# Kernel optimization log

Measured on AMD Instinct MI355X. Metric: run time of the kernel, lower is better.

The kernel has to match this reference:

```python
import jax, jax.numpy as jnp
import numpy as np


@jax.custom_vjp
def binarize(w):
    # Deterministic binarization: sign with ties (w==0) mapped to +1,
    # matching tf.where(w >= 0, 1.0, -1.0).
    return jnp.where(w >= 0, 1.0, -1.0).astype(w.dtype)


def _binarize_fwd(w):
    return binarize(w), w


def _binarize_bwd(w, g):
    # Straight-through estimator: pass grad where |w| < 1, else 0.
    return (jnp.where(jnp.abs(w) < 1.0, g, jnp.zeros_like(g)),)


binarize.defvjp(_binarize_fwd, _binarize_bwd)


def setup_inputs() -> dict:
    key = jax.random.key(0)
    kx, kw = jax.random.split(key)
    # NHWC activations
    x = jax.random.normal(kx, (32, 112, 112, 128), dtype=jnp.float32)
    # HWIO kernel (glorot-scale init so values straddle the +/- decision boundary)
    kernel = jax.random.normal(kw, (3, 3, 128, 256), dtype=jnp.float32) * 0.05
    return {"x": x, "kernel": kernel}


def reference(x, kernel):
    wb = binarize(kernel)  # [3,3,Cin,Cout] in {-1,+1}
    return jax.lax.conv_general_dilated(
        x, wb,
        window_strides=(1, 1),
        padding="SAME",
        dimension_numbers=("NHWC", "HWIO", "NHWC"),
    )
```

## Files before the change

### kernel.cpp

```cpp
#include <hip/hip_runtime.h>

typedef __attribute__((ext_vector_type(8))) short short8;
typedef __attribute__((ext_vector_type(4))) float f32x4;
typedef __attribute__((ext_vector_type(4))) unsigned short u16x4;
typedef __attribute__((ext_vector_type(8))) unsigned short u16x8;

#define H 112
#define W 112
#define HP 114
#define WP 114
#define CIN 128
#define COUT 256
#define NPIX (H * W)
#define NIMG 32
#define MTOT (NIMG * NPIX)
#define PADELEMS ((long)NIMG * HP * WP * CIN)
#define NKT 18

__device__ __forceinline__ unsigned short f2bf(float f) {
    unsigned int u = __builtin_bit_cast(unsigned int, f);
    u += 0x7FFFu + ((u >> 16) & 1u);
    return (unsigned short)(u >> 16);
}

__device__ __forceinline__ void gl2lds16(const void* g, void* l) {
    __builtin_amdgcn_global_load_lds(
        (const __attribute__((address_space(1))) unsigned int*)g,
        (__attribute__((address_space(3))) unsigned int*)l,
        16, 0, 0);
}

__global__ void binw2_kernel(const float* __restrict__ kw, unsigned short* __restrict__ bw) {
    int tid = blockIdx.x * 256 + threadIdx.x;
    int c    = tid & 63;
    int cout = (tid >> 6) & 255;
    int kh   = (tid >> 14) & 1;
    int tap  = tid >> 15;
    int cin  = kh * 64 + c;
    float w = kw[(tap * 128 + cin) * 256 + cout];
    bw[tid] = (w >= 0.0f) ? (unsigned short)0x3F80u : (unsigned short)0xBF80u;
}

__global__ void pad_kernel(const float* __restrict__ x, unsigned short* __restrict__ xp) {
    long tid = (long)blockIdx.x * 256 + threadIdx.x;
    if (tid >= PADELEMS / 8) return;
    int c8 = (int)(tid & 15);
    long rem = tid >> 4;
    int wp = (int)(rem % WP); rem /= WP;
    int hp = (int)(rem % HP);
    int n  = (int)(rem / HP);
    u16x8 v = {0, 0, 0, 0, 0, 0, 0, 0};
    if (hp >= 1 && hp <= H && wp >= 1 && wp <= W) {
        const float* s = x + (((long)(n * H + hp - 1) * W + (wp - 1)) * CIN + c8 * 8);
        f32x4 a = *(const f32x4*)s;
        f32x4 b = *(const f32x4*)(s + 4);
        v = (u16x8){ f2bf(a.x), f2bf(a.y), f2bf(a.z), f2bf(a.w),
                     f2bf(b.x), f2bf(b.y), f2bf(b.z), f2bf(b.w) };
    }
    *(u16x8*)(xp + tid * 8) = v;
}

__global__ __launch_bounds__(512, 2)
void conv3_kernel(const unsigned short* __restrict__ xp, const unsigned short* __restrict__ bw,
                  float* __restrict__ out) {
    __shared__ unsigned short As[2][256 * 64];
    __shared__ unsigned short Bs[2][256 * 64];

    const int tid = threadIdx.x;
    const int bm = (blockIdx.x & 7) * 196 + (blockIdx.x >> 3);
    const int lane = tid & 63;
    const int wv = tid >> 6;
    const int wr = wv >> 2;
    const int wc = wv & 3;

    const int r0 = tid >> 3;
    const int c8 = (tid & 7) ^ (r0 & 7);
    long apix[4];
#pragma unroll
    for (int j = 0; j < 4; ++j) {
        int row = r0 + j * 64;
        int p = bm * 256 + row;
        int n = p / NPIX;
        int rem = p - n * NPIX;
        int oh = rem / W, ow = rem - oh * W;
        apix[j] = (long)((n * HP + oh + 1) * WP + (ow + 1)) * CIN;
    }

#define STAGE(T1, BUF) do {                                                     \
        const int _tap = (T1) >> 1, _kh = (T1) & 1;                             \
        const long _sh = (long)((_tap / 3 - 1) * WP + (_tap % 3 - 1)) * CIN     \
                         + _kh * 64 + c8 * 8;                                   \
        const unsigned short* _bb = bw + ((_tap * 2 + _kh) << 14)               \
                                    + r0 * 64 + c8 * 8;                         \
        _Pragma("unroll")                                                       \
        for (int j = 0; j < 4; ++j)                                             \
            gl2lds16(xp + apix[j] + _sh, &As[BUF][(j * 512 + wv * 64) * 8]);    \
        _Pragma("unroll")                                                       \
        for (int j = 0; j < 4; ++j)                                             \
            gl2lds16(_bb + j * 4096, &Bs[BUF][(j * 512 + wv * 64) * 8]);        \
    } while (0)

    const int l15 = lane & 15;
    const int lq16 = (lane >> 4) * 16;
    const int arow0 = wr * 128 + l15;
    const int aswz = (arow0 & 7) << 4;
    const int abase = arow0 * 128 + lq16;
    const int brow0 = wc * 64 + l15;
    const int bswz = (brow0 & 7) << 4;
    const int bbase = brow0 * 128 + lq16;

    f32x4 acc[8][4];
#pragma unroll
    for (int m = 0; m < 8; ++m)
#pragma unroll
        for (int n = 0; n < 4; ++n)
            acc[m][n] = (f32x4){0.f, 0.f, 0.f, 0.f};

    STAGE(0, 0);

    short8 bfrag[4][2];
    for (int t = 0; t < NKT; ++t) {
        const int cur = t & 1;
        if (t < NKT - 1) {
            STAGE(t + 1, cur ^ 1);
            asm volatile("s_waitcnt vmcnt(8)" ::: "memory");
        } else {
            asm volatile("s_waitcnt vmcnt(0)" ::: "memory");
        }
        __builtin_amdgcn_s_barrier();

        const char* ab = (const char*)&As[cur][0];
        const char* bb = (const char*)&Bs[cur][0];
#pragma unroll
        for (int p = 0; p < 4; ++p) {
            if (p == 0) {
#pragma unroll
                for (int n = 0; n < 4; ++n)
#pragma unroll
                    for (int kk = 0; kk < 2; ++kk)
                        bfrag[n][kk] = *(const short8*)(bb + ((bbase + n * 2048 + kk * 64) ^ bswz));
            }
            short8 afr[2][2];
#pragma unroll
            for (int mi = 0; mi < 2; ++mi)
#pragma unroll
                for (int kk = 0; kk < 2; ++kk)
                    afr[mi][kk] = *(const short8*)(ab + ((abase + (2 * p + mi) * 2048 + kk * 64) ^ aswz));

            __builtin_amdgcn_s_setprio(1);
#pragma unroll
            for (int mi = 0; mi < 2; ++mi)
#pragma unroll
                for (int n = 0; n < 4; ++n)
#pragma unroll
                    for (int kk = 0; kk < 2; ++kk)
                        acc[2 * p + mi][n] = __builtin_amdgcn_mfma_f32_16x16x32_bf16(
                            afr[mi][kk], bfrag[n][kk], acc[2 * p + mi][n], 0, 0, 0);
            __builtin_amdgcn_s_setprio(0);
            __builtin_amdgcn_s_barrier();
        }
    }
#undef STAGE

    const long row0 = (long)bm * 256 + wr * 128 + (lane >> 4) * 4;
    const int col = wc * 64 + (lane & 15);
#pragma unroll
    for (int m = 0; m < 8; ++m)
#pragma unroll
        for (int n = 0; n < 4; ++n)
#pragma unroll
            for (int j = 0; j < 4; ++j)
                out[(row0 + m * 16 + j) * COUT + col + n * 16] = acc[m][n][j];
}

__global__ void binw_kernel(const float* __restrict__ kw, unsigned short* __restrict__ bw) {
    int tid = blockIdx.x * 256 + threadIdx.x;
    int cin5 = tid & 31;
    int cout = (tid >> 5) & 255;
    int kc4  = (tid >> 13) & 3;
    int tap  = tid >> 15;
    int cin  = kc4 * 32 + cin5;
    float w = kw[(tap * 128 + cin) * 256 + cout];
    bw[tid] = (w >= 0.0f) ? (unsigned short)0x3F80u : (unsigned short)0xBF80u;
}

__global__ __launch_bounds__(256, 2)
void conv_fallback_kernel(const float* __restrict__ x, const unsigned short* __restrict__ bw,
                          float* __restrict__ out) {
    __shared__ unsigned short As[128][40];
    __shared__ unsigned short Bs[128][40];
    const int tid = threadIdx.x;
    const int bm = blockIdx.x, bn = blockIdx.y;
    const int lane = tid & 63;
    const int wv = tid >> 6;
    const int wr = wv >> 1, wc = wv & 1;
    const int c4 = (tid & 7) * 4;
    const int rseg = tid >> 3;
    int ohs[4], ows[4], bases[4];
#pragma unroll
    for (int i = 0; i < 4; ++i) {
        int p = bm * 128 + rseg + i * 32;
        int n = p / NPIX;
        int rem = p - n * NPIX;
        int oh = rem / W, ow = rem - oh * W;
        ohs[i] = oh; ows[i] = ow;
        bases[i] = ((n * H + oh) * W + ow) * CIN;
    }
    f32x4 acc[4][4];
#pragma unroll
    for (int m = 0; m < 4; ++m)
#pragma unroll
        for (int n = 0; n < 4; ++n)
            acc[m][n] = (f32x4){0.f, 0.f, 0.f, 0.f};
    const int arow = wr * 64 + (lane & 15);
    const int brow = wc * 64 + (lane & 15);
    const int koff = (lane >> 4) * 8;
    for (int tap = 0; tap < 9; ++tap) {
        const int dh = tap / 3 - 1, dw = tap % 3 - 1;
        const int shift = (dh * W + dw) * CIN;
#pragma unroll
        for (int kc = 0; kc < 4; ++kc) {
            __syncthreads();
#pragma unroll
            for (int i = 0; i < 4; ++i) {
                int ih = ohs[i] + dh, iw = ows[i] + dw;
                bool valid = ((unsigned)ih < (unsigned)H) & ((unsigned)iw < (unsigned)W);
                f32x4 v = {0.f, 0.f, 0.f, 0.f};
                if (valid) v = *(const f32x4*)(x + bases[i] + shift + kc * 32 + c4);
                u16x4 s = { f2bf(v.x), f2bf(v.y), f2bf(v.z), f2bf(v.w) };
                *(u16x4*)&As[rseg + i * 32][c4] = s;
            }
            const unsigned short* bp = bw + tap * 32768 + kc * 8192 + bn * 4096;
#pragma unroll
            for (int j = 0; j < 2; ++j) {
                int idx = tid + j * 256;
                *(u16x8*)&Bs[idx >> 2][(idx & 3) * 8] = *(const u16x8*)(bp + (idx >> 2) * 32 + (idx & 3) * 8);
            }
            __syncthreads();
            short8 af[4], bfr[4];
#pragma unroll
            for (int m = 0; m < 4; ++m)
                af[m] = *(const short8*)&As[arow + m * 16][koff];
#pragma unroll
            for (int n = 0; n < 4; ++n)
                bfr[n] = *(const short8*)&Bs[brow + n * 16][koff];
#pragma unroll
            for (int m = 0; m < 4; ++m)
#pragma unroll
                for (int n = 0; n < 4; ++n)
                    acc[m][n] = __builtin_amdgcn_mfma_f32_16x16x32_bf16(af[m], bfr[n], acc[m][n], 0, 0, 0);
        }
    }
    const long row0 = (long)bm * 128 + wr * 64 + ((lane >> 4) * 4);
    const int col = bn * 128 + wc * 64 + (lane & 15);
#pragma unroll
    for (int m = 0; m < 4; ++m)
#pragma unroll
        for (int n = 0; n < 4; ++n)
#pragma unroll
            for (int j = 0; j < 4; ++j)
                out[(row0 + m * 16 + j) * COUT + col + n * 16] = acc[m][n][j];
}

extern "C" void kernel_launch(void* const* d_in, const int* in_sizes, int n_in,
                              void* d_out, int out_size, void* d_ws, size_t ws_size,
                              hipStream_t stream) {
    const float* x  = (const float*)d_in[0];
    const float* kw = (const float*)d_in[1];
    float* out = (float*)d_out;
    unsigned short* bw = (unsigned short*)d_ws;
    const size_t BW_BYTES = 9 * 2 * 256 * 64 * 2;
    const size_t PAD_BYTES = (size_t)PADELEMS * 2;

    if (ws_size >= BW_BYTES + PAD_BYTES) {
        binw2_kernel<<<(9 * 2 * 256 * 64) / 256, 256, 0, stream>>>(kw, bw);
        unsigned short* xp = (unsigned short*)((char*)d_ws + BW_BYTES);
        pad_kernel<<<(int)((PADELEMS / 8 + 255) / 256), 256, 0, stream>>>(x, xp);
        conv3_kernel<<<MTOT / 256, 512, 0, stream>>>(xp, bw, out);
    } else {
        binw_kernel<<<(9 * 256 * 128) / 256, 256, 0, stream>>>(kw, bw);
        dim3 grid(MTOT / 128, COUT / 128);
        conv_fallback_kernel<<<grid, 256, 0, stream>>>(x, bw, out);
    }
}
```

Before: 395.3 us.

## Interleave next-tile global-to-LDS loads across MFMA sub-phases in conv kernel

Splits the per-iteration prefetch of the next K tile into four quarters, each issued inside one of the four MFMA sub-phases, instead of issuing all loads at the top of the iteration. The last iteration is peeled and runs without prefetch or extra barriers. Explicit lgkmcnt waits and sched_barrier pin down instruction order. The goal is to spread memory traffic and hide load latency behind compute. The risk is extra scheduling constraints and barriers that could stall the waves.

```diff
diff --git a/kernel.cpp b/kernel.cpp
--- a/kernel.cpp
+++ b/kernel.cpp
@@ -61,7 +61,7 @@
 }
 
 __global__ __launch_bounds__(512, 2)
-void conv3_kernel(const unsigned short* __restrict__ xp, const unsigned short* __restrict__ bw,
+void conv4_kernel(const unsigned short* __restrict__ xp, const unsigned short* __restrict__ bw,
                   float* __restrict__ out) {
     __shared__ unsigned short As[2][256 * 64];
     __shared__ unsigned short Bs[2][256 * 64];
@@ -86,18 +86,13 @@
         apix[j] = (long)((n * HP + oh + 1) * WP + (ow + 1)) * CIN;
     }
 
-#define STAGE(T1, BUF) do {                                                     \
+#define STAGE_HALF(T1, BUF, J) do {                                             \
         const int _tap = (T1) >> 1, _kh = (T1) & 1;                             \
         const long _sh = (long)((_tap / 3 - 1) * WP + (_tap % 3 - 1)) * CIN     \
                          + _kh * 64 + c8 * 8;                                   \
-        const unsigned short* _bb = bw + ((_tap * 2 + _kh) << 14)               \
-                                    + r0 * 64 + c8 * 8;                         \
-        _Pragma("unroll")                                                       \
-        for (int j = 0; j < 4; ++j)                                             \
-            gl2lds16(xp + apix[j] + _sh, &As[BUF][(j * 512 + wv * 64) * 8]);    \
-        _Pragma("unroll")                                                       \
-        for (int j = 0; j < 4; ++j)                                             \
-            gl2lds16(_bb + j * 4096, &Bs[BUF][(j * 512 + wv * 64) * 8]);        \
+        gl2lds16(xp + apix[J] + _sh, &As[BUF][((J) * 512 + wv * 64) * 8]);      \
+        gl2lds16(bw + ((_tap * 2 + _kh) << 14) + r0 * 64 + c8 * 8 + (J) * 4096, \
+                 &Bs[BUF][((J) * 512 + wv * 64) * 8]);                          \
     } while (0)
 
     const int l15 = lane & 15;
@@ -116,37 +111,45 @@
         for (int n = 0; n < 4; ++n)
             acc[m][n] = (f32x4){0.f, 0.f, 0.f, 0.f};
 
-    STAGE(0, 0);
-
-    short8 bfrag[4][2];
-    for (int t = 0; t < NKT; ++t) {
+    STAGE_HALF(0, 0, 0);
+    STAGE_HALF(0, 0, 1);
+    STAGE_HALF(0, 0, 2);
+    STAGE_HALF(0, 0, 3);
+
+    for (int t = 0; t < NKT - 1; ++t) {
         const int cur = t & 1;
-        if (t < NKT - 1) {
-            STAGE(t + 1, cur ^ 1);
-            asm volatile("s_waitcnt vmcnt(8)" ::: "memory");
-        } else {
-            asm volatile("s_waitcnt vmcnt(0)" ::: "memory");
-        }
-        __builtin_amdgcn_s_barrier();
-
+        const int nxt = cur ^ 1;
         const char* ab = (const char*)&As[cur][0];
         const char* bb = (const char*)&Bs[cur][0];
+        short8 bfrag[4][2];
 #pragma unroll
         for (int p = 0; p < 4; ++p) {
+            short8 afr[2][2];
             if (p == 0) {
+                STAGE_HALF(t + 1, nxt, 0);
+                asm volatile("s_waitcnt vmcnt(2)" ::: "memory");
+                __builtin_amdgcn_s_barrier();
 #pragma unroll
                 for (int n = 0; n < 4; ++n)
 #pragma unroll
                     for (int kk = 0; kk < 2; ++kk)
                         bfrag[n][kk] = *(const short8*)(bb + ((bbase + n * 2048 + kk * 64) ^ bswz));
+#pragma unroll
+                for (int mi = 0; mi < 2; ++mi)
+#pragma unroll
+                    for (int kk = 0; kk < 2; ++kk)
+                        afr[mi][kk] = *(const short8*)(ab + ((abase + mi * 2048 + kk * 64) ^ aswz));
+            } else {
+#pragma unroll
+                for (int mi = 0; mi < 2; ++mi)
+#pragma unroll
+                    for (int kk = 0; kk < 2; ++kk)
+                        afr[mi][kk] = *(const short8*)(ab + ((abase + (2 * p + mi) * 2048 + kk * 64) ^ aswz));
+                STAGE_HALF(t + 1, nxt, p);
+                __builtin_amdgcn_s_barrier();
             }
-            short8 afr[2][2];
-#pragma unroll
-            for (int mi = 0; mi < 2; ++mi)
-#pragma unroll
-                for (int kk = 0; kk < 2; ++kk)
-                    afr[mi][kk] = *(const short8*)(ab + ((abase + (2 * p + mi) * 2048 + kk * 64) ^ aswz));
-
+            asm volatile("s_waitcnt lgkmcnt(0)" ::: "memory");
+            __builtin_amdgcn_sched_barrier(0);
             __builtin_amdgcn_s_setprio(1);
 #pragma unroll
             for (int mi = 0; mi < 2; ++mi)
@@ -160,7 +163,38 @@
             __builtin_amdgcn_s_barrier();
         }
     }
-#undef STAGE
+
+    {
+        const int cur = (NKT - 1) & 1;
+        const char* ab = (const char*)&As[cur][0];
+        const char* bb = (const char*)&Bs[cur][0];
+        asm volatile("s_waitcnt vmcnt(0)" ::: "memory");
+        __builtin_amdgcn_s_barrier();
+        short8 bfrag[4][2];
+#pragma unroll
+        for (int n = 0; n < 4; ++n)
+#pragma unroll
+            for (int kk = 0; kk < 2; ++kk)
+                bfrag[n][kk] = *(const short8*)(bb + ((bbase + n * 2048 + kk * 64) ^ bswz));
+#pragma unroll
+        for (int p = 0; p < 4; ++p) {
+            short8 afr[2][2];
+#pragma unroll
+            for (int mi = 0; mi < 2; ++mi)
+#pragma unroll
+                for (int kk = 0; kk < 2; ++kk)
+                    afr[mi][kk] = *(const short8*)(ab + ((abase + (2 * p + mi) * 2048 + kk * 64) ^ aswz));
+#pragma unroll
+            for (int mi = 0; mi < 2; ++mi)
+#pragma unroll
+                for (int n = 0; n < 4; ++n)
+#pragma unroll
+                    for (int kk = 0; kk < 2; ++kk)
+                        acc[2 * p + mi][n] = __builtin_amdgcn_mfma_f32_16x16x32_bf16(
+                            afr[mi][kk], bfrag[n][kk], acc[2 * p + mi][n], 0, 0, 0);
+        }
+    }
+#undef STAGE_HALF
 
     const long row0 = (long)bm * 256 + wr * 128 + (lane >> 4) * 4;
     const int col = wc * 64 + (lane & 15);
@@ -276,7 +310,7 @@
         binw2_kernel<<<(9 * 2 * 256 * 64) / 256, 256, 0, stream>>>(kw, bw);
         unsigned short* xp = (unsigned short*)((char*)d_ws + BW_BYTES);
         pad_kernel<<<(int)((PADELEMS / 8 + 255) / 256), 256, 0, stream>>>(x, xp);
-        conv3_kernel<<<MTOT / 256, 512, 0, stream>>>(xp, bw, out);
+        conv4_kernel<<<MTOT / 256, 512, 0, stream>>>(xp, bw, out);
     } else {
         binw_kernel<<<(9 * 256 * 128) / 256, 256, 0, stream>>>(kw, bw);
         dim3 grid(MTOT / 128, COUT / 128);
```

After: 360.1 us. 1.1x faster.

## Switch conv GEMM to 32x32x16 MFMA with k-plane LDS layout

Applied to the files above, without the earlier changes.

Replaces the 16x16x32 bf16 MFMA tiling with 32x32x16 MFMA tiles (4x2 per wave) and reorganizes LDS so each 8-channel slice is stored as its own plane across 256 rows. The intent is to cut LDS fragment reads per MFMA and drop the XOR swizzle in favor of a simpler plane layout, while fully unrolling the K loop and removing the per-subtile barriers and priority hints. It risks LDS bank conflicts from the unswizzled layout and higher register pressure from the fully unrolled loop.

```diff
diff --git a/kernel.cpp b/kernel.cpp
--- a/kernel.cpp
+++ b/kernel.cpp
@@ -2,6 +2,7 @@
 
 typedef __attribute__((ext_vector_type(8))) short short8;
 typedef __attribute__((ext_vector_type(4))) float f32x4;
+typedef __attribute__((ext_vector_type(16))) float f32x16;
 typedef __attribute__((ext_vector_type(4))) unsigned short u16x4;
 typedef __attribute__((ext_vector_type(8))) unsigned short u16x8;
 
@@ -28,6 +29,13 @@
         (const __attribute__((address_space(1))) unsigned int*)g,
         (__attribute__((address_space(3))) unsigned int*)l,
         16, 0, 0);
+}
+
+__device__ __forceinline__ int pidx(int p) {
+    int n = p / NPIX;
+    int r = p - n * NPIX;
+    int oh = r / W, ow = r - oh * W;
+    return n * (HP * WP) + (oh + 1) * WP + ow + 1;
 }
 
 __global__ void binw2_kernel(const float* __restrict__ kw, unsigned short* __restrict__ bw) {
@@ -61,10 +69,10 @@
 }
 
 __global__ __launch_bounds__(512, 2)
-void conv3_kernel(const unsigned short* __restrict__ xp, const unsigned short* __restrict__ bw,
-                  float* __restrict__ out) {
-    __shared__ unsigned short As[2][256 * 64];
-    __shared__ unsigned short Bs[2][256 * 64];
+void conv11_kernel(const unsigned short* __restrict__ xp, const unsigned short* __restrict__ bw,
+                   float* __restrict__ out) {
+    __shared__ unsigned short As[2][8 * 256 * 8];
+    __shared__ unsigned short Bs[2][8 * 256 * 8];
 
     const int tid = threadIdx.x;
     const int bm = (blockIdx.x & 7) * 196 + (blockIdx.x >> 3);
@@ -72,105 +80,86 @@
     const int wv = tid >> 6;
     const int wr = wv >> 2;
     const int wc = wv & 3;
-
-    const int r0 = tid >> 3;
-    const int c8 = (tid & 7) ^ (r0 & 7);
-    long apix[4];
-#pragma unroll
-    for (int j = 0; j < 4; ++j) {
-        int row = r0 + j * 64;
-        int p = bm * 256 + row;
-        int n = p / NPIX;
-        int rem = p - n * NPIX;
-        int oh = rem / W, ow = rem - oh * W;
-        apix[j] = (long)((n * HP + oh + 1) * WP + (ow + 1)) * CIN;
-    }
-
-#define STAGE(T1, BUF) do {                                                     \
-        const int _tap = (T1) >> 1, _kh = (T1) & 1;                             \
-        const long _sh = (long)((_tap / 3 - 1) * WP + (_tap % 3 - 1)) * CIN     \
-                         + _kh * 64 + c8 * 8;                                   \
-        const unsigned short* _bb = bw + ((_tap * 2 + _kh) << 14)               \
-                                    + r0 * 64 + c8 * 8;                         \
+    const int l31 = lane & 31;
+    const int lh = lane >> 5;
+
+    const int srow = tid & 255;
+    const int sp0 = tid >> 8;
+    const unsigned short* aptr = xp + (long)pidx(bm * 256 + srow) * CIN;
+    const unsigned short* bptr = bw + srow * 64;
+
+#define STAGE(T, BUF) do {                                                      \
+        const int _tap = (T) >> 1, _kh = (T) & 1;                               \
+        const int _sh = ((_tap / 3 - 1) * WP + (_tap % 3 - 1)) * CIN            \
+                        + _kh * 64;                                             \
+        const unsigned short* _bb = bptr + (((_tap * 2 + _kh)) << 14);          \
         _Pragma("unroll")                                                       \
-        for (int j = 0; j < 4; ++j)                                             \
-            gl2lds16(xp + apix[j] + _sh, &As[BUF][(j * 512 + wv * 64) * 8]);    \
-        _Pragma("unroll")                                                       \
-        for (int j = 0; j < 4; ++j)                                             \
-            gl2lds16(_bb + j * 4096, &Bs[BUF][(j * 512 + wv * 64) * 8]);        \
+        for (int j = 0; j < 4; ++j) {                                           \
+            const int _pl = sp0 + 2 * j;                                        \
+            gl2lds16(aptr + _sh + _pl * 8,                                      \
+                     &As[BUF][((_pl) * 256 + srow) * 8]);                       \
+            gl2lds16(_bb + _pl * 8,                                             \
+                     &Bs[BUF][((_pl) * 256 + srow) * 8]);                       \
+        }                                                                       \
     } while (0)
 
-    const int l15 = lane & 15;
-    const int lq16 = (lane >> 4) * 16;
-    const int arow0 = wr * 128 + l15;
-    const int aswz = (arow0 & 7) << 4;
-    const int abase = arow0 * 128 + lq16;
-    const int brow0 = wc * 64 + l15;
-    const int bswz = (brow0 & 7) << 4;
-    const int bbase = brow0 * 128 + lq16;
-
-    f32x4 acc[8][4];
-#pragma unroll
-    for (int m = 0; m < 8; ++m)
-#pragma unroll
-        for (int n = 0; n < 4; ++n)
-            acc[m][n] = (f32x4){0.f, 0.f, 0.f, 0.f};
+    const int afr0 = lh * 2048 + (wr * 128 + l31) * 8;
+    const int bfr0 = lh * 2048 + (wc * 64 + l31) * 8;
+
+    f32x16 acc[4][2];
+#pragma unroll
+    for (int mt = 0; mt < 4; ++mt)
+#pragma unroll
+        for (int nt = 0; nt < 2; ++nt)
+            acc[mt][nt] = (f32x16){0.f,0.f,0.f,0.f,0.f,0.f,0.f,0.f,
+                                   0.f,0.f,0.f,0.f,0.f,0.f,0.f,0.f};
 
     STAGE(0, 0);
 
-    short8 bfrag[4][2];
+#pragma unroll
     for (int t = 0; t < NKT; ++t) {
-        const int cur = t & 1;
+        const int buf = t & 1;
         if (t < NKT - 1) {
-            STAGE(t + 1, cur ^ 1);
+            STAGE(t + 1, buf ^ 1);
             asm volatile("s_waitcnt vmcnt(8)" ::: "memory");
         } else {
             asm volatile("s_waitcnt vmcnt(0)" ::: "memory");
         }
         __builtin_amdgcn_s_barrier();
 
-        const char* ab = (const char*)&As[cur][0];
-        const char* bb = (const char*)&Bs[cur][0];
-#pragma unroll
-        for (int p = 0; p < 4; ++p) {
-            if (p == 0) {
-#pragma unroll
-                for (int n = 0; n < 4; ++n)
-#pragma unroll
-                    for (int kk = 0; kk < 2; ++kk)
-                        bfrag[n][kk] = *(const short8*)(bb + ((bbase + n * 2048 + kk * 64) ^ bswz));
+        const unsigned short* a = &As[buf][0];
+        const unsigned short* b = &Bs[buf][0];
+#pragma unroll
+        for (int ks = 0; ks < 4; ++ks) {
+            short8 bfr[2], afr[4];
+#pragma unroll
+            for (int nt = 0; nt < 2; ++nt)
+                bfr[nt] = *(const short8*)(b + bfr0 + ks * 4096 + nt * 256);
+#pragma unroll
+            for (int mt = 0; mt < 4; ++mt)
+                afr[mt] = *(const short8*)(a + afr0 + ks * 4096 + mt * 256);
+#pragma unroll
+            for (int mt = 0; mt < 4; ++mt)
+#pragma unroll
+                for (int nt = 0; nt < 2; ++nt)
+                    acc[mt][nt] = __builtin_amdgcn_mfma_f32_32x32x16_bf16(
+                        afr[mt], bfr[nt], acc[mt][nt], 0, 0, 0);
+        }
+        __builtin_amdgcn_s_barrier();
+    }
+#undef STAGE
+
+    const long rbase = (long)bm * 256 + wr * 128 + 4 * lh;
+    const int cbase = wc * 64 + l31;
+#pragma unroll
+    for (int mt = 0; mt < 4; ++mt)
+#pragma unroll
+        for (int nt = 0; nt < 2; ++nt)
+#pragma unroll
+            for (int r = 0; r < 16; ++r) {
+                long row = rbase + mt * 32 + (r & 3) + 8 * (r >> 2);
+                out[row * COUT + cbase + nt * 32] = acc[mt][nt][r];
             }
-            short8 afr[2][2];
-#pragma unroll
-            for (int mi = 0; mi < 2; ++mi)
-#pragma unroll
-                for (int kk = 0; kk < 2; ++kk)
-                    afr[mi][kk] = *(const short8*)(ab + ((abase + (2 * p + mi) * 2048 + kk * 64) ^ aswz));
-
-            __builtin_amdgcn_s_setprio(1);
-#pragma unroll
-            for (int mi = 0; mi < 2; ++mi)
-#pragma unroll
-                for (int n = 0; n < 4; ++n)
-#pragma unroll
-                    for (int kk = 0; kk < 2; ++kk)
-                        acc[2 * p + mi][n] = __builtin_amdgcn_mfma_f32_16x16x32_bf16(
-                            afr[mi][kk], bfrag[n][kk], acc[2 * p + mi][n], 0, 0, 0);
-            __builtin_amdgcn_s_setprio(0);
-            __builtin_amdgcn_s_barrier();
-        }
-    }
-#undef STAGE
-
-    const long row0 = (long)bm * 256 + wr * 128 + (lane >> 4) * 4;
-    const int col = wc * 64 + (lane & 15);
-#pragma unroll
-    for (int m = 0; m < 8; ++m)
-#pragma unroll
-        for (int n = 0; n < 4; ++n)
-#pragma unroll
-            for (int j = 0; j < 4; ++j)
-                out[(row0 + m * 16 + j) * COUT + col + n * 16] = acc[m][n][j];
 }
 
 __global__ void binw_kernel(const float* __restrict__ kw, unsigned short* __restrict__ bw) {
@@ -276,7 +265,7 @@
         binw2_kernel<<<(9 * 2 * 256 * 64) / 256, 256, 0, stream>>>(kw, bw);
         unsigned short* xp = (unsigned short*)((char*)d_ws + BW_BYTES);
         pad_kernel<<<(int)((PADELEMS / 8 + 255) / 256), 256, 0, stream>>>(x, xp);
-        conv3_kernel<<<MTOT / 256, 512, 0, stream>>>(xp, bw, out);
+        conv11_kernel<<<MTOT / 256, 512, 0, stream>>>(xp, bw, out);
     } else {
         binw_kernel<<<(9 * 256 * 128) / 256, 256, 0, stream>>>(kw, bw);
         dim3 grid(MTOT / 128, COUT / 128);
```

Result: slower. 621.0 us (+57.1%).
